# Performance work log

Measured on AMD Instinct MI355X. Metric: run time of the kernel, lower is better.

Reference implementation:

```python
import jax, jax.numpy as jnp
import numpy as np
from jax import lax

N = 100000          # nodes
E = 1600000         # directed edges (before self loops)
NODE_DIM = 64       # input feature dim (== hidden so layer weights stack)
C = 64              # out_channels per head
H = 4               # attention heads
L = 3               # layers
NEG_SLOPE = 0.2     # GATv2 leaky_relu slope
EPS = 1e-5          # LayerNorm eps


def setup_inputs() -> dict:
    key = jax.random.key(0)
    ks = jax.random.split(key, 8)
    s = 0.05
    x = jax.random.normal(ks[0], (N, NODE_DIM), jnp.float32)
    edge_index = jax.random.randint(ks[1], (2, E), 0, N, dtype=jnp.int32)
    # GATv2Conv params per layer (concat=False): lin_l, lin_r, att, bias
    Wl = jax.random.normal(ks[2], (L, NODE_DIM, H * C), jnp.float32) * s
    Wr = jax.random.normal(ks[3], (L, NODE_DIM, H * C), jnp.float32) * s
    att = jax.random.normal(ks[4], (L, H, C), jnp.float32) * s
    bias = jnp.zeros((L, C), jnp.float32)
    # PyG LayerNorm affine params
    ln_w = jnp.ones((L, C), jnp.float32)
    ln_b = jnp.zeros((L, C), jnp.float32)
    return {"x": x, "edge_index": edge_index, "Wl": Wl, "Wr": Wr,
            "att": att, "bias": bias, "ln_w": ln_w, "ln_b": ln_b}


def _gatv2_layer(x, src, dst, Wl, Wr, att, bias):
    # x: [N, D]; src/dst: [E'] (self loops included)
    xl = (x @ Wl).reshape(N, H, C)          # source transform
    xr = (x @ Wr).reshape(N, H, C)          # target transform
    # GATv2 attention: a^T LeakyReLU(xl_j + xr_i)
    e = jax.nn.leaky_relu(xl[src] + xr[dst], NEG_SLOPE)   # [E', H, C]
    logits = jnp.einsum("ehc,hc->eh", e, att)             # [E', H]
    # numerically stable scatter-softmax over incoming edges of each dst node
    m = jax.ops.segment_max(logits, dst, num_segments=N)  # [N, H]
    ex = jnp.exp(logits - lax.stop_gradient(m)[dst])
    denom = jax.ops.segment_sum(ex, dst, num_segments=N)  # [N, H]
    alpha = ex / (denom[dst] + 1e-16)                     # [E', H]
    out = jax.ops.segment_sum(alpha[:, :, None] * xl[src], dst, num_segments=N)
    return out.mean(axis=1) + bias                        # concat=False -> head mean


def _graph_layernorm(x, w, b):
    # PyG LayerNorm default mode='graph': normalize over all nodes & features
    mu = jnp.mean(x)
    var = jnp.mean((x - mu) ** 2)
    return (x - mu) * lax.rsqrt(var + EPS) * w + b


def reference(x, edge_index, Wl, Wr, att, bias, ln_w, ln_b):
    # add self loops once (GATv2Conv default add_self_loops=True)
    loop = jnp.arange(N, dtype=edge_index.dtype)
    src = jnp.concatenate([edge_index[0], loop])
    dst = jnp.concatenate([edge_index[1], loop])
    for i in range(L):
        x = _gatv2_layer(x, src, dst, Wl[i], Wr[i], att[i], bias[i])
        x = _graph_layernorm(x, ln_w[i], ln_b[i])
        # dropout p=0.0 -> identity (eval reference)
    return x
```

## Files before the change

kernel.cpp:

```cpp
#include <hip/hip_runtime.h>
#include <hip/hip_bf16.h>

#define HEADS 4
#define NEG 0.2f
#define LN_EPS 1e-5f
#define LOG2E 1.4426950408889634f
#define C06 (0.6f * LOG2E)
#define C04 (0.4f * LOG2E)

typedef unsigned int u32;
typedef unsigned short u16;

typedef __attribute__((ext_vector_type(8))) short bf16x8;
typedef __attribute__((ext_vector_type(4))) float f32x4;
typedef __attribute__((ext_vector_type(2))) float f32x2;

__device__ __forceinline__ float bflo(u32 u) { return __uint_as_float(u << 16); }
__device__ __forceinline__ float bfhi(u32 u) { return __uint_as_float(u & 0xffff0000u); }
__device__ __forceinline__ u16 f2bf(float f) {
    u32 u = __float_as_uint(f);
    u32 r = u + 0x7fffu + ((u >> 16) & 1u);
    return (u16)(r >> 16);
}

template <int CTRL>
__device__ __forceinline__ float dppadd(float e) {
    float t = __int_as_float(
        __builtin_amdgcn_update_dpp(0, __float_as_int(e), CTRL, 0xf, 0xf, false));
    return e + t;
}
__device__ __forceinline__ float redsum8(float e) {
    e = dppadd<0xB1>(e);
    e = dppadd<0x4E>(e);
    e = dppadd<0x141>(e);
    return e;
}
__device__ __forceinline__ float rowsum16(float e) {
    e = dppadd<0x128>(e);
    e = dppadd<0x124>(e);
    e = dppadd<0x122>(e);
    e = dppadd<0x121>(e);
    return e;
}

__device__ __forceinline__ f32x2 pk_fma(f32x2 a, f32x2 b, f32x2 c) {
    f32x2 d;
    asm("v_pk_fma_f32 %0, %1, %2, %3" : "=v"(d) : "v"(a), "v"(b), "v"(c));
    return d;
}
__device__ __forceinline__ f32x2 pk_add(f32x2 a, f32x2 b) {
    f32x2 d;
    asm("v_pk_add_f32 %0, %1, %2" : "=v"(d) : "v"(a), "v"(b));
    return d;
}

#define BSH 9
#define BSZ 512

__global__ void k_init(int* bcur, int nbuck16, float* buckets) {
    int i = blockIdx.x * blockDim.x + threadIdx.x;
    if (i < nbuck16) bcur[i] = 0;
    if (i < 1024) buckets[i] = 0.f;
}

__global__ void k_bucketA(const int* __restrict__ src, const int* __restrict__ dst,
                          int* __restrict__ bcur, uint2* __restrict__ stage,
                          int E, int cap) {
    int stride = gridDim.x * blockDim.x;
    for (int e = blockIdx.x * blockDim.x + threadIdx.x; e < E; e += stride) {
        int s = src[e], d = dst[e];
        int b = d >> BSH;
        int pos = atomicAdd(&bcur[b * 16], 1);
        if (pos < cap) stage[(size_t)b * cap + pos] = make_uint2((u32)s, (u32)d);
    }
}

__global__ void k_bcount(const int* __restrict__ bcur, const uint2* __restrict__ stage,
                         int* __restrict__ cnt, int n, int cap) {
    __shared__ int hist[BSZ];
    int b = blockIdx.x;
    int base = b << BSH;
    for (int i = threadIdx.x; i < BSZ; i += 256) hist[i] = 1;
    __syncthreads();
    int c = min(bcur[b * 16], cap);
    const uint2* sp = stage + (size_t)b * cap;
    for (int i = threadIdx.x; i < c; i += 256)
        atomicAdd(&hist[(int)sp[i].y - base], 1);
    __syncthreads();
    for (int i = threadIdx.x; i < BSZ; i += 256)
        if (base + i < n) cnt[base + i] = hist[i];
}

__global__ void k_blocksum(const int* __restrict__ cnt, int* bsum, int n) {
    __shared__ int sh[256];
    int i = blockIdx.x * 256 + threadIdx.x;
    int v = (i < n) ? cnt[i] : 0;
    sh[threadIdx.x] = v;
    __syncthreads();
    for (int off = 128; off; off >>= 1) {
        if (threadIdx.x < off) sh[threadIdx.x] += sh[threadIdx.x + off];
        __syncthreads();
    }
    if (threadIdx.x == 0) bsum[blockIdx.x] = sh[0];
}

__global__ void k_scan_bsum(const int* __restrict__ bsum, int* boff, int nb) {
    __shared__ int sh[1024];
    int t = threadIdx.x;
    int v = (t < nb) ? bsum[t] : 0;
    sh[t] = v;
    __syncthreads();
    for (int off = 1; off < 1024; off <<= 1) {
        int a = (t >= off) ? sh[t - off] : 0;
        __syncthreads();
        sh[t] += a;
        __syncthreads();
    }
    if (t < nb) boff[t] = sh[t] - v;
}

__global__ void k_make_ptr(const int* cnt, const int* __restrict__ boff,
                           int* rowptr, int n) {
    __shared__ int sh[256];
    int t = threadIdx.x;
    int i = blockIdx.x * 256 + t;
    int v = (i < n) ? cnt[i] : 0;
    sh[t] = v;
    __syncthreads();
    for (int off = 1; off < 256; off <<= 1) {
        int a = (t >= off) ? sh[t - off] : 0;
        __syncthreads();
        sh[t] += a;
        __syncthreads();
    }
    int incl = sh[t] + boff[blockIdx.x];
    if (i < n) rowptr[i + 1] = incl;
    if (i == 0) rowptr[0] = 0;
}

__global__ void k_bfill(const int* __restrict__ bcur, const uint2* __restrict__ stage,
                        const int* __restrict__ rowptr, int* __restrict__ col_src,
                        int n, int cap) {
    __shared__ int lcur[BSZ];
    int b = blockIdx.x;
    int base = b << BSH;
    for (int i = threadIdx.x; i < BSZ; i += 256) {
        if (base + i < n) {
            int rp = rowptr[base + i];
            col_src[rp] = base + i;
            lcur[i] = rp + 1;
        }
    }
    __syncthreads();
    int c = min(bcur[b * 16], cap);
    const uint2* sp = stage + (size_t)b * cap;
    for (int i = threadIdx.x; i < c; i += 256) {
        uint2 e = sp[i];
        int p = atomicAdd(&lcur[(int)e.y - base], 1);
        col_src[p] = (int)e.x;
    }
}

__global__ void k_prep_w(const float* __restrict__ Wl, const float* __restrict__ Wr,
                         u16* __restrict__ wt) {
    int idx = blockIdx.x * 256 + threadIdx.x;
    if (idx >= 6 * 16384) return;
    int mat = idx >> 14;
    int rem = idx & 16383;
    int t = rem >> 10;
    int kq = (rem >> 8) & 3;
    int nn = (rem >> 4) & 15;
    int half = (rem >> 3) & 1;
    int j = rem & 7;
    int c = t * 16 + nn;
    int k = kq * 8 + half * 32 + j;
    const float* W = (mat < 3) ? (Wl + (size_t)mat * 16384) : (Wr + (size_t)(mat - 3) * 16384);
    wt[idx] = f2bf(W[k * 256 + c]);
}

__global__ __launch_bounds__(256) void k_gemm_mfma(
        const float* __restrict__ x, const u16* __restrict__ wtl,
        const u16* __restrict__ wtr, u16* __restrict__ xl, u16* __restrict__ xr,
        float* __restrict__ ALs, float* __restrict__ ARs,
        const float* __restrict__ att, int n,
        const float* __restrict__ musig, const float* __restrict__ lnw,
        const float* __restrict__ lnb, int useln) {
    int w = threadIdx.x >> 6;
    int lane = threadIdx.x & 63;
    int r = blockIdx.x * 64 + w * 16 + (lane & 15);
    int c0 = (lane >> 4) * 8;

    float mu = 0.f, rs = 1.f;
    if (useln) { mu = musig[0]; rs = musig[1]; }

    float av[16];
    if (r < n) {
        const float* xp = x + (size_t)r * 64;
        float4 t0 = *(const float4*)(xp + c0);
        float4 t1 = *(const float4*)(xp + c0 + 4);
        float4 t2 = *(const float4*)(xp + c0 + 32);
        float4 t3 = *(const float4*)(xp + c0 + 36);
        av[0] = t0.x; av[1] = t0.y; av[2] = t0.z; av[3] = t0.w;
        av[4] = t1.x; av[5] = t1.y; av[6] = t1.z; av[7] = t1.w;
        av[8] = t2.x; av[9] = t2.y; av[10] = t2.z; av[11] = t2.w;
        av[12] = t3.x; av[13] = t3.y; av[14] = t3.z; av[15] = t3.w;
        if (useln) {
            float4 w0 = *(const float4*)(lnw + c0);
            float4 w1 = *(const float4*)(lnw + c0 + 4);
            float4 w2 = *(const float4*)(lnw + c0 + 32);
            float4 w3 = *(const float4*)(lnw + c0 + 36);
            float4 b0 = *(const float4*)(lnb + c0);
            float4 b1 = *(const float4*)(lnb + c0 + 4);
            float4 b2 = *(const float4*)(lnb + c0 + 32);
            float4 b3 = *(const float4*)(lnb + c0 + 36);
            float lw[16] = {w0.x,w0.y,w0.z,w0.w, w1.x,w1.y,w1.z,w1.w,
                            w2.x,w2.y,w2.z,w2.w, w3.x,w3.y,w3.z,w3.w};
            float lb[16] = {b0.x,b0.y,b0.z,b0.w, b1.x,b1.y,b1.z,b1.w,
                            b2.x,b2.y,b2.z,b2.w, b3.x,b3.y,b3.z,b3.w};
#pragma unroll
            for (int j = 0; j < 16; ++j) av[j] = (av[j] - mu) * rs * lw[j] + lb[j];
        }
    } else {
#pragma unroll
        for (int j = 0; j < 16; ++j) av[j] = 0.f;
    }
    bf16x8 fa0, fa1;
#pragma unroll
    for (int j = 0; j < 8; ++j) {
        fa0[j] = (short)f2bf(av[j]);
        fa1[j] = (short)f2bf(av[8 + j]);
    }

    int nn = lane & 15;
    int kq = lane >> 4;
    int row0 = blockIdx.x * 64 + w * 16 + kq * 4;
    int fragoff = kq * 256 + nn * 16;

    float pal[4] = {0.f, 0.f, 0.f, 0.f};
#pragma unroll 4
    for (int t = 0; t < 16; ++t) {
        const u16* wp = wtl + t * 1024 + fragoff;
        bf16x8 fb0 = *(const bf16x8*)(wp);
        bf16x8 fb1 = *(const bf16x8*)(wp + 8);
        f32x4 acc = {0.f, 0.f, 0.f, 0.f};
        acc = __builtin_amdgcn_mfma_f32_16x16x32_bf16(fa0, fb0, acc, 0, 0, 0);
        acc = __builtin_amdgcn_mfma_f32_16x16x32_bf16(fa1, fb1, acc, 0, 0, 0);
        int cb = t * 16;
        float attv = att[cb + nn];
#pragma unroll
        for (int reg = 0; reg < 4; ++reg) {
            int R = row0 + reg;
            if (R < n) xl[(size_t)R * 256 + cb + nn] = f2bf(acc[reg]);
            pal[reg] = fmaf(attv, acc[reg], pal[reg]);
        }
        if ((t & 3) == 3) {
            int h = t >> 2;
#pragma unroll
            for (int reg = 0; reg < 4; ++reg) {
                float s = rowsum16(pal[reg]);
                if (nn == 0) {
                    int R = row0 + reg;
                    if (R < n) ALs[(size_t)R * 4 + h] = s * C06;
                }
                pal[reg] = 0.f;
            }
        }
    }
#pragma unroll 4
    for (int t = 0; t < 16; ++t) {
        const u16* wp = wtr + t * 1024 + fragoff;
        bf16x8 fb0 = *(const bf16x8*)(wp);
        bf16x8 fb1 = *(const bf16x8*)(wp + 8);
        f32x4 acc = {0.f, 0.f, 0.f, 0.f};
        acc = __builtin_amdgcn_mfma_f32_16x16x32_bf16(fa0, fb0, acc, 0, 0, 0);
        acc = __builtin_amdgcn_mfma_f32_16x16x32_bf16(fa1, fb1, acc, 0, 0, 0);
        int cb = t * 16;
        float attv = att[cb + nn];
#pragma unroll
        for (int reg = 0; reg < 4; ++reg) {
            int R = row0 + reg;
            if (R < n) xr[(size_t)R * 256 + cb + nn] = f2bf(acc[reg]);
            pal[reg] = fmaf(attv, acc[reg], pal[reg]);
        }
        if ((t & 3) == 3) {
            int h = t >> 2;
#pragma unroll
            for (int reg = 0; reg < 4; ++reg) {
                float s = rowsum16(pal[reg]);
                if (nn == 0) {
                    int R = row0 + reg;
                    if (R < n) ARs[(size_t)R * 4 + h] = s * C06;
                }
                pal[reg] = 0.f;
            }
        }
    }
}

__global__ __launch_bounds__(256) void k_fused(
        const u16* __restrict__ xl, const u16* __restrict__ xr,
        const float* __restrict__ ALs, const float* __restrict__ ARs,
        const int* __restrict__ rowptr, const int* __restrict__ col_src,
        const float* __restrict__ att, const float* __restrict__ bias,
        float* __restrict__ y, float* __restrict__ buckets, int n) {
    __shared__ float shv[4][HEADS][64];
    __shared__ float redS[4], redQ[4];
    int w = threadIdx.x >> 6;
    int node = blockIdx.x * 4 + w;
    int lane = threadIdx.x & 63;
    int half = lane >> 5;
    int l32 = lane & 31;
    int h = l32 >> 3;
    bool act = node < n;
    float yv = 0.f;

    if (act) {
        f32x2 at0, at1, at2, at3, rr0, rr1, rr2, rr3;
        {
            const float* ap = att + l32 * 8;
            float4 a0 = *(const float4*)(ap);
            float4 a1 = *(const float4*)(ap + 4);
            at0 = (f32x2){a0.x * C04, a0.y * C04};
            at1 = (f32x2){a0.z * C04, a0.w * C04};
            at2 = (f32x2){a1.x * C04, a1.y * C04};
            at3 = (f32x2){a1.z * C04, a1.w * C04};
            uint4 rv = *(const uint4*)(xr + (size_t)node * 256 + l32 * 8);
            rr0 = (f32x2){bflo(rv.x), bfhi(rv.x)};
            rr1 = (f32x2){bflo(rv.y), bfhi(rv.y)};
            rr2 = (f32x2){bflo(rv.z), bfhi(rv.z)};
            rr3 = (f32x2){bflo(rv.w), bfhi(rv.w)};
        }
        float base_d = ARs[(size_t)node * 4 + h];
        int start = rowptr[node], end = rowptr[node + 1];
        int d = end - start;
        int iters = (d + 1) >> 1;
        f32x2 acc0 = {0.f, 0.f}, acc1 = {0.f, 0.f}, acc2 = {0.f, 0.f}, acc3 = {0.f, 0.f};
        f32x2 z2 = {0.f, 0.f};
        float denom = 0.f;
        int j = start + half;
        const size_t co = (size_t)l32 * 8;
        uint4 v;
        float af;
        {
            int jc = min(j, end - 1);
            int s = col_src[jc];
            v = *(const uint4*)(xl + (size_t)s * 256 + co);
            af = ALs[(size_t)s * 4 + h];
        }
        for (int i = 0; i < iters; ++i) {
            uint4 vc = v;
            float afc = af;
            bool valid = j < end;
            int jn = j + 2;
            if (i + 1 < iters) {
                int jnc = min(jn, end - 1);
                int sn = col_src[jnc];
                v = *(const uint4*)(xl + (size_t)sn * 256 + co);
                af = ALs[(size_t)sn * 4 + h];
            }
            f32x2 x0 = {bflo(vc.x), bfhi(vc.x)};
            f32x2 x1 = {bflo(vc.y), bfhi(vc.y)};
            f32x2 x2 = {bflo(vc.z), bfhi(vc.z)};
            f32x2 x3 = {bflo(vc.w), bfhi(vc.w)};
            f32x2 u0 = pk_add(x0, rr0);
            f32x2 u1 = pk_add(x1, rr1);
            f32x2 u2 = pk_add(x2, rr2);
            f32x2 u3 = pk_add(x3, rr3);
            f32x2 au0 = {__builtin_fabsf(u0.x), __builtin_fabsf(u0.y)};
            f32x2 au1 = {__builtin_fabsf(u1.x), __builtin_fabsf(u1.y)};
            f32x2 au2 = {__builtin_fabsf(u2.x), __builtin_fabsf(u2.y)};
            f32x2 au3 = {__builtin_fabsf(u3.x), __builtin_fabsf(u3.y)};
            f32x2 red = pk_fma(at0, au0, z2);
            red = pk_fma(at1, au1, red);
            red = pk_fma(at2, au2, red);
            red = pk_fma(at3, au3, red);
            float e = red.x + red.y;
            e = redsum8(e);
            float e2 = e + afc + base_d;
            float p = exp2f(e2);
            p = valid ? p : 0.f;
            denom += p;
            f32x2 pp = {p, p};
            acc0 = pk_fma(pp, x0, acc0);
            acc1 = pk_fma(pp, x1, acc1);
            acc2 = pk_fma(pp, x2, acc2);
            acc3 = pk_fma(pp, x3, acc3);
            j = jn;
        }
        acc0.x += __shfl_xor(acc0.x, 32, 64); acc0.y += __shfl_xor(acc0.y, 32, 64);
        acc1.x += __shfl_xor(acc1.x, 32, 64); acc1.y += __shfl_xor(acc1.y, 32, 64);
        acc2.x += __shfl_xor(acc2.x, 32, 64); acc2.y += __shfl_xor(acc2.y, 32, 64);
        acc3.x += __shfl_xor(acc3.x, 32, 64); acc3.y += __shfl_xor(acc3.y, 32, 64);
        denom += __shfl_xor(denom, 32, 64);
        float invd = 0.25f / (denom + 1e-16f);
        if (half == 0) {
            int cb = (l32 & 7) * 8;
            shv[w][h][cb + 0] = acc0.x * invd;
            shv[w][h][cb + 1] = acc0.y * invd;
            shv[w][h][cb + 2] = acc1.x * invd;
            shv[w][h][cb + 3] = acc1.y * invd;
            shv[w][h][cb + 4] = acc2.x * invd;
            shv[w][h][cb + 5] = acc2.y * invd;
            shv[w][h][cb + 6] = acc3.x * invd;
            shv[w][h][cb + 7] = acc3.y * invd;
        }
        yv = shv[w][0][lane] + shv[w][1][lane] + shv[w][2][lane] + shv[w][3][lane]
             + bias[lane];
        y[(size_t)node * 64 + lane] = yv;
    }

    float s1 = yv, s2 = yv * yv;
#pragma unroll
    for (int off = 32; off; off >>= 1) {
        s1 += __shfl_xor(s1, off, 64);
        s2 += __shfl_xor(s2, off, 64);
    }
    if (lane == 0) { redS[w] = act ? s1 : 0.f; redQ[w] = act ? s2 : 0.f; }
    __syncthreads();
    if (threadIdx.x == 0) {
        float bs = redS[0] + redS[1] + redS[2] + redS[3];
        float bq = redQ[0] + redQ[1] + redQ[2] + redQ[3];
        int b = blockIdx.x & 511;
        atomicAdd(&buckets[b], bs);
        atomicAdd(&buckets[512 + b], bq);
    }
}

__global__ void k_ln_final(float* __restrict__ buckets, float* musig, int n64) {
    int t = threadIdx.x;
    double s = (double)buckets[t];
    double q = (double)buckets[512 + t];
    __shared__ double shs[512], shq[512];
    shs[t] = s; shq[t] = q;
    __syncthreads();
    for (int off = 256; off; off >>= 1) {
        if (t < off) { shs[t] += shs[t + off]; shq[t] += shq[t + off]; }
        __syncthreads();
    }
    if (t == 0) {
        double mu = shs[0] / n64;
        double var = shq[0] / n64 - mu * mu;
        musig[0] = (float)mu;
        musig[1] = (float)(1.0 / sqrt(var + (double)LN_EPS));
    }
    buckets[t] = 0.f;
    buckets[512 + t] = 0.f;
}

__global__ void k_ln_apply(const float* __restrict__ y, const float* __restrict__ musig,
                           const float* __restrict__ w, const float* __restrict__ b,
                           float* __restrict__ out, int n64) {
    float mu = musig[0], rs = musig[1];
    int stride = gridDim.x * blockDim.x;
    for (int i = blockIdx.x * blockDim.x + threadIdx.x; i < n64; i += stride) {
        int c = i & 63;
        out[i] = (y[i] - mu) * rs * w[c] + b[c];
    }
}

extern "C" void kernel_launch(void* const* d_in, const int* in_sizes, int n_in,
                              void* d_out, int out_size, void* d_ws, size_t ws_size,
                              hipStream_t stream) {
    const float* x0   = (const float*)d_in[0];
    const int*   ei   = (const int*)d_in[1];
    const float* Wl   = (const float*)d_in[2];
    const float* Wr   = (const float*)d_in[3];
    const float* att  = (const float*)d_in[4];
    const float* bias = (const float*)d_in[5];
    const float* lnw  = (const float*)d_in[6];
    const float* lnb  = (const float*)d_in[7];

    const int n  = in_sizes[0] / 64;
    const int E  = in_sizes[1] / 2;
    const int* srcA = ei;
    const int* dstA = ei + E;

    const int NBUCK = (n + BSZ - 1) >> BSH;
    const int cap = ((E / NBUCK) * 5 / 4 + 512 + 63) & ~63;

    char* p = (char*)d_ws;
    auto alloc = [&](size_t bytes) -> char* {
        char* r = p;
        p += (bytes + 511) & ~((size_t)511);
        return r;
    };
    u16*    xl      = (u16*)alloc((size_t)n * 256 * 2);
    u16*    xr      = (u16*)alloc((size_t)n * 256 * 2);
    float*  ybuf    = (float*)alloc((size_t)n * 64 * 4);
    float*  ALs     = (float*)alloc((size_t)n * 4 * 4);
    float*  ARs     = (float*)alloc((size_t)n * 4 * 4);
    int*    rowptr  = (int*)alloc((size_t)(n + 1) * 4);
    int*    cnt     = (int*)alloc((size_t)n * 4);
    const int nb    = (n + 255) / 256;
    int*    bsum    = (int*)alloc((size_t)nb * 4);
    int*    boff    = (int*)alloc((size_t)nb * 4);
    int*    col_src = (int*)alloc((size_t)(E + n) * 4);
    int*    bcur    = (int*)alloc((size_t)NBUCK * 16 * 4);
    uint2*  stage   = (uint2*)alloc((size_t)NBUCK * cap * 8);
    u16*    wt      = (u16*)alloc((size_t)6 * 16384 * 2);
    float*  buckets = (float*)alloc(1024 * 4);
    float*  musig   = (float*)alloc(16);

    k_init<<<(n + 255) / 256, 256, 0, stream>>>(bcur, NBUCK * 16, buckets);
    k_bucketA<<<2048, 256, 0, stream>>>(srcA, dstA, bcur, stage, E, cap);
    k_bcount<<<NBUCK, 256, 0, stream>>>(bcur, stage, cnt, n, cap);
    k_blocksum<<<nb, 256, 0, stream>>>(cnt, bsum, n);
    k_scan_bsum<<<1, 1024, 0, stream>>>(bsum, boff, nb);
    k_make_ptr<<<nb, 256, 0, stream>>>(cnt, boff, rowptr, n);
    k_bfill<<<NBUCK, 256, 0, stream>>>(bcur, stage, rowptr, col_src, n, cap);
    k_prep_w<<<(6 * 16384 + 255) / 256, 256, 0, stream>>>(Wl, Wr, wt);

    for (int l = 0; l < 3; ++l) {
        const float* xin = (l == 0) ? x0 : ybuf;
        k_gemm_mfma<<<(n + 63) / 64, 256, 0, stream>>>(
            xin, wt + (size_t)l * 16384, wt + (size_t)(3 + l) * 16384, xl, xr,
            ALs, ARs, att + l * 256, n,
            musig, lnw + (l - 1) * 64, lnb + (l - 1) * 64, l > 0 ? 1 : 0);
        k_fused<<<(n + 3) / 4, 256, 0, stream>>>(
            xl, xr, ALs, ARs, rowptr, col_src, att + l * 256, bias + l * 64,
            ybuf, buckets, n);
        k_ln_final<<<1, 512, 0, stream>>>(buckets, musig, n * 64);
    }
    k_ln_apply<<<2048, 256, 0, stream>>>(ybuf, musig, lnw + 2 * 64, lnb + 2 * 64,
                                         (float*)d_out, n * 64);
}
```

Baseline: 806.0 us.

## Compute full leaky-relu logit per edge and split bucket counters into sub-buckets

The attention logit was previously decomposed as 0.6*a·(xl+xr) + 0.4*a·|xl+xr|, with the linear parts precomputed per node in the GEMM kernel and gathered per edge. Now the edge kernel computes both the linear and absolute-value terms directly, so the GEMM no longer does the per-head reductions and the edge loop drops an extra scalar gather, at the price of more packed FMAs per edge. Separately, the edge bucketing now spreads each bucket's atomic counter over 8 sub-buckets, chosen by block index, to reduce atomic contention. The counting and fill kernels loop over these sub-buckets, and the per-sub-bucket capacity changes accordingly.

```diff
diff --git a/kernel.cpp b/kernel.cpp
--- a/kernel.cpp
+++ b/kernel.cpp
@@ -5,8 +5,6 @@
 #define NEG 0.2f
 #define LN_EPS 1e-5f
 #define LOG2E 1.4426950408889634f
-#define C06 (0.6f * LOG2E)
-#define C04 (0.4f * LOG2E)
 
 typedef unsigned int u32;
 typedef unsigned short u16;
@@ -35,13 +33,6 @@
     e = dppadd<0x141>(e);
     return e;
 }
-__device__ __forceinline__ float rowsum16(float e) {
-    e = dppadd<0x128>(e);
-    e = dppadd<0x124>(e);
-    e = dppadd<0x122>(e);
-    e = dppadd<0x121>(e);
-    return e;
-}
 
 __device__ __forceinline__ f32x2 pk_fma(f32x2 a, f32x2 b, f32x2 c) {
     f32x2 d;
@@ -56,36 +47,42 @@
 
 #define BSH 9
 #define BSZ 512
-
-__global__ void k_init(int* bcur, int nbuck16, float* buckets) {
+#define NSUB 8
+
+__global__ void k_init(int* bcur, int ncur, float* buckets) {
     int i = blockIdx.x * blockDim.x + threadIdx.x;
-    if (i < nbuck16) bcur[i] = 0;
+    if (i < ncur) bcur[i] = 0;
     if (i < 1024) buckets[i] = 0.f;
 }
 
 __global__ void k_bucketA(const int* __restrict__ src, const int* __restrict__ dst,
                           int* __restrict__ bcur, uint2* __restrict__ stage,
-                          int E, int cap) {
+                          int E, int subcap) {
+    int sub = blockIdx.x & (NSUB - 1);
     int stride = gridDim.x * blockDim.x;
     for (int e = blockIdx.x * blockDim.x + threadIdx.x; e < E; e += stride) {
         int s = src[e], d = dst[e];
         int b = d >> BSH;
-        int pos = atomicAdd(&bcur[b * 16], 1);
-        if (pos < cap) stage[(size_t)b * cap + pos] = make_uint2((u32)s, (u32)d);
+        int st = b * NSUB + sub;
+        int pos = atomicAdd(&bcur[st * 16], 1);
+        if (pos < subcap) stage[(size_t)st * subcap + pos] = make_uint2((u32)s, (u32)d);
     }
 }
 
 __global__ void k_bcount(const int* __restrict__ bcur, const uint2* __restrict__ stage,
-                         int* __restrict__ cnt, int n, int cap) {
+                         int* __restrict__ cnt, int n, int subcap) {
     __shared__ int hist[BSZ];
     int b = blockIdx.x;
     int base = b << BSH;
     for (int i = threadIdx.x; i < BSZ; i += 256) hist[i] = 1;
     __syncthreads();
-    int c = min(bcur[b * 16], cap);
-    const uint2* sp = stage + (size_t)b * cap;
-    for (int i = threadIdx.x; i < c; i += 256)
-        atomicAdd(&hist[(int)sp[i].y - base], 1);
+    for (int ss = 0; ss < NSUB; ++ss) {
+        int st = b * NSUB + ss;
+        int c = min(bcur[st * 16], subcap);
+        const uint2* sp = stage + (size_t)st * subcap;
+        for (int i = threadIdx.x; i < c; i += 256)
+            atomicAdd(&hist[(int)sp[i].y - base], 1);
+    }
     __syncthreads();
     for (int i = threadIdx.x; i < BSZ; i += 256)
         if (base + i < n) cnt[base + i] = hist[i];
@@ -140,7 +137,7 @@
 
 __global__ void k_bfill(const int* __restrict__ bcur, const uint2* __restrict__ stage,
                         const int* __restrict__ rowptr, int* __restrict__ col_src,
-                        int n, int cap) {
+                        int n, int subcap) {
     __shared__ int lcur[BSZ];
     int b = blockIdx.x;
     int base = b << BSH;
@@ -152,12 +149,15 @@
         }
     }
     __syncthreads();
-    int c = min(bcur[b * 16], cap);
-    const uint2* sp = stage + (size_t)b * cap;
-    for (int i = threadIdx.x; i < c; i += 256) {
-        uint2 e = sp[i];
-        int p = atomicAdd(&lcur[(int)e.y - base], 1);
-        col_src[p] = (int)e.x;
+    for (int ss = 0; ss < NSUB; ++ss) {
+        int st = b * NSUB + ss;
+        int c = min(bcur[st * 16], subcap);
+        const uint2* sp = stage + (size_t)st * subcap;
+        for (int i = threadIdx.x; i < c; i += 256) {
+            uint2 e = sp[i];
+            int p = atomicAdd(&lcur[(int)e.y - base], 1);
+            col_src[p] = (int)e.x;
+        }
     }
 }
 
@@ -180,9 +180,7 @@
 
 __global__ __launch_bounds__(256) void k_gemm_mfma(
         const float* __restrict__ x, const u16* __restrict__ wtl,
-        const u16* __restrict__ wtr, u16* __restrict__ xl, u16* __restrict__ xr,
-        float* __restrict__ ALs, float* __restrict__ ARs,
-        const float* __restrict__ att, int n,
+        const u16* __restrict__ wtr, u16* __restrict__ xl, u16* __restrict__ xr, int n,
         const float* __restrict__ musig, const float* __restrict__ lnw,
         const float* __restrict__ lnb, int useln) {
     int w = threadIdx.x >> 6;
@@ -236,7 +234,6 @@
     int row0 = blockIdx.x * 64 + w * 16 + kq * 4;
     int fragoff = kq * 256 + nn * 16;
 
-    float pal[4] = {0.f, 0.f, 0.f, 0.f};
 #pragma unroll 4
     for (int t = 0; t < 16; ++t) {
         const u16* wp = wtl + t * 1024 + fragoff;
@@ -246,24 +243,10 @@
         acc = __builtin_amdgcn_mfma_f32_16x16x32_bf16(fa0, fb0, acc, 0, 0, 0);
         acc = __builtin_amdgcn_mfma_f32_16x16x32_bf16(fa1, fb1, acc, 0, 0, 0);
         int cb = t * 16;
-        float attv = att[cb + nn];
 #pragma unroll
         for (int reg = 0; reg < 4; ++reg) {
             int R = row0 + reg;
             if (R < n) xl[(size_t)R * 256 + cb + nn] = f2bf(acc[reg]);
-            pal[reg] = fmaf(attv, acc[reg], pal[reg]);
-        }
-        if ((t & 3) == 3) {
-            int h = t >> 2;
-#pragma unroll
-            for (int reg = 0; reg < 4; ++reg) {
-                float s = rowsum16(pal[reg]);
-                if (nn == 0) {
-                    int R = row0 + reg;
-                    if (R < n) ALs[(size_t)R * 4 + h] = s * C06;
-                }
-                pal[reg] = 0.f;
-            }
         }
     }
 #pragma unroll 4
@@ -275,31 +258,16 @@
         acc = __builtin_amdgcn_mfma_f32_16x16x32_bf16(fa0, fb0, acc, 0, 0, 0);
         acc = __builtin_amdgcn_mfma_f32_16x16x32_bf16(fa1, fb1, acc, 0, 0, 0);
         int cb = t * 16;
-        float attv = att[cb + nn];
 #pragma unroll
         for (int reg = 0; reg < 4; ++reg) {
             int R = row0 + reg;
             if (R < n) xr[(size_t)R * 256 + cb + nn] = f2bf(acc[reg]);
-            pal[reg] = fmaf(attv, acc[reg], pal[reg]);
-        }
-        if ((t & 3) == 3) {
-            int h = t >> 2;
-#pragma unroll
-            for (int reg = 0; reg < 4; ++reg) {
-                float s = rowsum16(pal[reg]);
-                if (nn == 0) {
-                    int R = row0 + reg;
-                    if (R < n) ARs[(size_t)R * 4 + h] = s * C06;
-                }
-                pal[reg] = 0.f;
-            }
         }
     }
 }
 
 __global__ __launch_bounds__(256) void k_fused(
         const u16* __restrict__ xl, const u16* __restrict__ xr,
-        const float* __restrict__ ALs, const float* __restrict__ ARs,
         const int* __restrict__ rowptr, const int* __restrict__ col_src,
         const float* __restrict__ att, const float* __restrict__ bias,
         float* __restrict__ y, float* __restrict__ buckets, int n) {
@@ -315,22 +283,26 @@
     float yv = 0.f;
 
     if (act) {
-        f32x2 at0, at1, at2, at3, rr0, rr1, rr2, rr3;
+        f32x2 a60, a61, a62, a63, a40, a41, a42, a43, rr0, rr1, rr2, rr3;
         {
             const float* ap = att + l32 * 8;
             float4 a0 = *(const float4*)(ap);
             float4 a1 = *(const float4*)(ap + 4);
-            at0 = (f32x2){a0.x * C04, a0.y * C04};
-            at1 = (f32x2){a0.z * C04, a0.w * C04};
-            at2 = (f32x2){a1.x * C04, a1.y * C04};
-            at3 = (f32x2){a1.z * C04, a1.w * C04};
+            const float c6 = 0.6f * LOG2E, c4 = 0.4f * LOG2E;
+            a60 = (f32x2){a0.x * c6, a0.y * c6};
+            a61 = (f32x2){a0.z * c6, a0.w * c6};
+            a62 = (f32x2){a1.x * c6, a1.y * c6};
+            a63 = (f32x2){a1.z * c6, a1.w * c6};
+            a40 = (f32x2){a0.x * c4, a0.y * c4};
+            a41 = (f32x2){a0.z * c4, a0.w * c4};
+            a42 = (f32x2){a1.x * c4, a1.y * c4};
+            a43 = (f32x2){a1.z * c4, a1.w * c4};
             uint4 rv = *(const uint4*)(xr + (size_t)node * 256 + l32 * 8);
             rr0 = (f32x2){bflo(rv.x), bfhi(rv.x)};
             rr1 = (f32x2){bflo(rv.y), bfhi(rv.y)};
             rr2 = (f32x2){bflo(rv.z), bfhi(rv.z)};
             rr3 = (f32x2){bflo(rv.w), bfhi(rv.w)};
         }
-        float base_d = ARs[(size_t)node * 4 + h];
         int start = rowptr[node], end = rowptr[node + 1];
         int d = end - start;
         int iters = (d + 1) >> 1;
@@ -340,23 +312,19 @@
         int j = start + half;
         const size_t co = (size_t)l32 * 8;
         uint4 v;
-        float af;
         {
             int jc = min(j, end - 1);
             int s = col_src[jc];
             v = *(const uint4*)(xl + (size_t)s * 256 + co);
-            af = ALs[(size_t)s * 4 + h];
         }
         for (int i = 0; i < iters; ++i) {
             uint4 vc = v;
-            float afc = af;
             bool valid = j < end;
             int jn = j + 2;
             if (i + 1 < iters) {
                 int jnc = min(jn, end - 1);
                 int sn = col_src[jnc];
                 v = *(const uint4*)(xl + (size_t)sn * 256 + co);
-                af = ALs[(size_t)sn * 4 + h];
             }
             f32x2 x0 = {bflo(vc.x), bfhi(vc.x)};
             f32x2 x1 = {bflo(vc.y), bfhi(vc.y)};
@@ -366,18 +334,31 @@
             f32x2 u1 = pk_add(x1, rr1);
             f32x2 u2 = pk_add(x2, rr2);
             f32x2 u3 = pk_add(x3, rr3);
-            f32x2 au0 = {__builtin_fabsf(u0.x), __builtin_fabsf(u0.y)};
-            f32x2 au1 = {__builtin_fabsf(u1.x), __builtin_fabsf(u1.y)};
-            f32x2 au2 = {__builtin_fabsf(u2.x), __builtin_fabsf(u2.y)};
-            f32x2 au3 = {__builtin_fabsf(u3.x), __builtin_fabsf(u3.y)};
-            f32x2 red = pk_fma(at0, au0, z2);
-            red = pk_fma(at1, au1, red);
-            red = pk_fma(at2, au2, red);
-            red = pk_fma(at3, au3, red);
-            float e = red.x + red.y;
+            f32x2 redA = pk_fma(a60, u0, z2);
+            f32x2 redB;
+            {
+                f32x2 au0 = {__builtin_fabsf(u0.x), __builtin_fabsf(u0.y)};
+                redB = pk_fma(a40, au0, z2);
+            }
+            redA = pk_fma(a61, u1, redA);
+            {
+                f32x2 au1 = {__builtin_fabsf(u1.x), __builtin_fabsf(u1.y)};
+                redB = pk_fma(a41, au1, redB);
+            }
+            redA = pk_fma(a62, u2, redA);
+            {
+                f32x2 au2 = {__builtin_fabsf(u2.x), __builtin_fabsf(u2.y)};
+                redB = pk_fma(a42, au2, redB);
+            }
+            redA = pk_fma(a63, u3, redA);
+            {
+                f32x2 au3 = {__builtin_fabsf(u3.x), __builtin_fabsf(u3.y)};
+                redB = pk_fma(a43, au3, redB);
+            }
+            f32x2 rsum = pk_add(redA, redB);
+            float e = rsum.x + rsum.y;
             e = redsum8(e);
-            float e2 = e + afc + base_d;
-            float p = exp2f(e2);
+            float p = exp2f(e);
             p = valid ? p : 0.f;
             denom += p;
             f32x2 pp = {p, p};
@@ -476,7 +457,7 @@
     const int* dstA = ei + E;
 
     const int NBUCK = (n + BSZ - 1) >> BSH;
-    const int cap = ((E / NBUCK) * 5 / 4 + 512 + 63) & ~63;
+    const int subcap = ((E / (NBUCK * NSUB)) * 3 / 2 + 256 + 63) & ~63;
 
     char* p = (char*)d_ws;
     auto alloc = [&](size_t bytes) -> char* {
@@ -487,37 +468,34 @@
     u16*    xl      = (u16*)alloc((size_t)n * 256 * 2);
     u16*    xr      = (u16*)alloc((size_t)n * 256 * 2);
     float*  ybuf    = (float*)alloc((size_t)n * 64 * 4);
-    float*  ALs     = (float*)alloc((size_t)n * 4 * 4);
-    float*  ARs     = (float*)alloc((size_t)n * 4 * 4);
     int*    rowptr  = (int*)alloc((size_t)(n + 1) * 4);
     int*    cnt     = (int*)alloc((size_t)n * 4);
     const int nb    = (n + 255) / 256;
     int*    bsum    = (int*)alloc((size_t)nb * 4);
     int*    boff    = (int*)alloc((size_t)nb * 4);
     int*    col_src = (int*)alloc((size_t)(E + n) * 4);
-    int*    bcur    = (int*)alloc((size_t)NBUCK * 16 * 4);
-    uint2*  stage   = (uint2*)alloc((size_t)NBUCK * cap * 8);
+    int*    bcur    = (int*)alloc((size_t)NBUCK * NSUB * 16 * 4);
+    uint2*  stage   = (uint2*)alloc((size_t)NBUCK * NSUB * subcap * 8);
     u16*    wt      = (u16*)alloc((size_t)6 * 16384 * 2);
     float*  buckets = (float*)alloc(1024 * 4);
     float*  musig   = (float*)alloc(16);
 
-    k_init<<<(n + 255) / 256, 256, 0, stream>>>(bcur, NBUCK * 16, buckets);
-    k_bucketA<<<2048, 256, 0, stream>>>(srcA, dstA, bcur, stage, E, cap);
-    k_bcount<<<NBUCK, 256, 0, stream>>>(bcur, stage, cnt, n, cap);
+    k_init<<<(n + 255) / 256, 256, 0, stream>>>(bcur, NBUCK * NSUB * 16, buckets);
+    k_bucketA<<<2048, 256, 0, stream>>>(srcA, dstA, bcur, stage, E, subcap);
+    k_bcount<<<NBUCK, 256, 0, stream>>>(bcur, stage, cnt, n, subcap);
     k_blocksum<<<nb, 256, 0, stream>>>(cnt, bsum, n);
     k_scan_bsum<<<1, 1024, 0, stream>>>(bsum, boff, nb);
     k_make_ptr<<<nb, 256, 0, stream>>>(cnt, boff, rowptr, n);
-    k_bfill<<<NBUCK, 256, 0, stream>>>(bcur, stage, rowptr, col_src, n, cap);
+    k_bfill<<<NBUCK, 256, 0, stream>>>(bcur, stage, rowptr, col_src, n, subcap);
     k_prep_w<<<(6 * 16384 + 255) / 256, 256, 0, stream>>>(Wl, Wr, wt);
 
     for (int l = 0; l < 3; ++l) {
         const float* xin = (l == 0) ? x0 : ybuf;
         k_gemm_mfma<<<(n + 63) / 64, 256, 0, stream>>>(
-            xin, wt + (size_t)l * 16384, wt + (size_t)(3 + l) * 16384, xl, xr,
-            ALs, ARs, att + l * 256, n,
+            xin, wt + (size_t)l * 16384, wt + (size_t)(3 + l) * 16384, xl, xr, n,
             musig, lnw + (l - 1) * 64, lnb + (l - 1) * 64, l > 0 ? 1 : 0);
         k_fused<<<(n + 3) / 4, 256, 0, stream>>>(
-            xl, xr, ALs, ARs, rowptr, col_src, att + l * 256, bias + l * 64,
+            xl, xr, rowptr, col_src, att + l * 256, bias + l * 64,
             ybuf, buckets, n);
         k_ln_final<<<1, 512, 0, stream>>>(buckets, musig, n * 64);
     }
```

Result: faster. 683.6 us (-15.2%).
